# Optimization experiments

Hardware: AMD Instinct MI355X
Metric: run time of the kernel (lower is better)

Reference implementation:

```python
import jax, jax.numpy as jnp
import numpy as np

B, S, V, E, P, C = 256, 128, 32000, 300, 200, 3
DIST_CUTOFF = 10

def _seq_mask(x):
    # TF: count_nonzero over seq, sequence_mask, expand to [B, S, 1]
    size = jnp.sum(x != 0, axis=1)
    m = (jnp.arange(S)[None, :] < size[:, None]).astype(jnp.float32)
    return m[:, :, None]

def _l2norm(w):
    n = jnp.sqrt(jnp.maximum(jnp.sum(w * w, axis=-1, keepdims=True), 1e-12))
    return w / n

def setup_inputs() -> dict:
    key = jax.random.key(0)
    ks = jax.random.split(key, 11)
    std = 0.01
    x1 = jax.random.randint(ks[0], (B, S), 0, V, dtype=jnp.int32)
    x2 = jax.random.randint(ks[1], (B, S), 0, V, dtype=jnp.int32)
    emb = jax.random.normal(ks[2], (V, E), jnp.float32)
    w_intra = jax.random.normal(ks[3], (E, E), jnp.float32) * std
    bias_intra = jax.random.normal(ks[4], (1,), jnp.float32) * std
    w_proj1 = jax.random.normal(ks[5], (2 * E, P), jnp.float32) * std
    w_proj2 = jax.random.normal(ks[6], (2 * E, P), jnp.float32) * std
    w_att = jax.random.normal(ks[7], (P, P), jnp.float32) * std
    w_cmp1 = jax.random.normal(ks[8], (2 * P, 2 * P), jnp.float32) * std
    w_cmp2 = jax.random.normal(ks[9], (2 * P, 2 * P), jnp.float32) * std
    w_agg = jax.random.normal(ks[10], (4 * P, C), jnp.float32) * std
    return dict(x1=x1, x2=x2, emb=emb, w_intra=w_intra, bias_intra=bias_intra,
                w_proj1=w_proj1, w_proj2=w_proj2, w_att=w_att,
                w_cmp1=w_cmp1, w_cmp2=w_cmp2, w_agg=w_agg)

def reference(x1, x2, emb, w_intra, bias_intra, w_proj1, w_proj2, w_att, w_cmp1, w_cmp2, w_agg):
    relu = jax.nn.relu
    mask1, mask2 = _seq_mask(x1), _seq_mask(x2)  # [B,S,1]

    # normalized embedding lookup
    e = _l2norm(emb)
    e1, e2 = e[x1], e[x2]  # [B,S,E]

    # intra-attention with distance bias (bias zeroed for |i-j| < 10)
    idx = jnp.arange(S)
    dist = jnp.abs(idx[None, :] - idx[:, None])
    dbias = bias_intra[0] * (dist >= DIST_CUTOFF).astype(jnp.float32)  # [S,S]

    def intra(x):
        f = relu(x @ w_intra)                       # shared F, [B,S,E]
        att = jnp.einsum('bik,bjk->bij', f, f)      # [B,S,S]
        sm = jax.nn.softmax(att + dbias[None], axis=2)
        xp = jnp.einsum('bik,bkj->bij', sm, x)
        return jnp.concatenate([x, xp], axis=2)     # [B,S,2E]

    e1, e2 = intra(e1), intra(e2)

    # project
    x1p = relu(e1 @ w_proj1)  # [B,S,P]
    x2p = relu(e2 @ w_proj2)

    # attend: F(x1) . F(x2), multiplicative mask, two softmaxes
    f1 = relu(x1p @ w_att)
    f2 = relu(x2p @ w_att)
    sim = jnp.einsum('bik,bjk->bij', f1, f2)          # [B,S1,S2]
    sim = sim * (mask1 * jnp.swapaxes(mask2, 1, 2))   # multiplicative mask (as in source)
    alpha = jnp.einsum('bki,bkj->bij', jax.nn.softmax(sim, axis=1), x1p)  # [B,S2,P]
    beta = jnp.einsum('bik,bkj->bij', jax.nn.softmax(sim, axis=2), x2p)   # [B,S1,P]

    # compare
    v1 = relu(jnp.concatenate([x1p, beta], axis=2) @ w_cmp1)
    v2 = relu(jnp.concatenate([x2p, alpha], axis=2) @ w_cmp2)

    # aggregate (masked sum pooling) + final ReLU projection (faithful to source)
    v1 = jnp.sum(v1 * mask1, axis=1)
    v2 = jnp.sum(v2 * mask2, axis=1)
    y_hat = relu(jnp.concatenate([v1, v2], axis=1) @ w_agg)  # [B,C]
    return y_hat
```

## Files before the change

### kernel.cpp

```cpp
#include <hip/hip_runtime.h>

#define BATCH 256
#define SEQ   128
#define EDIM  300
#define PDIM  200
#define BSTOK (BATCH * SEQ)

#define F_RELU  1
#define F_ACCUM 2

typedef unsigned short u16;
typedef __attribute__((ext_vector_type(8))) short bf16x8;
typedef __attribute__((ext_vector_type(4))) float f32x4;

__device__ __forceinline__ u16 f2bf(float x) {
    unsigned u = __float_as_uint(x);
    unsigned r = u + 0x7fffu + ((u >> 16) & 1u);
    return (u16)(r >> 16);
}
__device__ __forceinline__ float bf2f(u16 h) {
    return __uint_as_float(((unsigned)h) << 16);
}

__device__ __forceinline__ unsigned char* swz16(unsigned char* base, int row, int chunk) {
    return base + row * 64 + (((chunk ^ (row >> 1)) & 3) << 4);
}

__device__ __forceinline__ void split_store8(const float* va,
    unsigned char* bH, unsigned char* bL, int row, int chunk)
{
    unsigned hp[4], lp[4];
    #pragma unroll
    for (int i = 0; i < 4; i++) {
        const unsigned u0 = __float_as_uint(va[2 * i]);
        const unsigned u1 = __float_as_uint(va[2 * i + 1]);
        const unsigned h0 = u0 & 0xffff0000u;
        const unsigned h1 = u1 & 0xffff0000u;
        hp[i] = (u0 >> 16) | h1;
        const float r0 = va[2 * i]     - __uint_as_float(h0);
        const float r1 = va[2 * i + 1] - __uint_as_float(h1);
        lp[i] = (__float_as_uint(r0) >> 16) | (__float_as_uint(r1) & 0xffff0000u);
    }
    *(uint4*)swz16(bH, row, chunk) = make_uint4(hp[0], hp[1], hp[2], hp[3]);
    *(uint4*)swz16(bL, row, chunk) = make_uint4(lp[0], lp[1], lp[2], lp[3]);
}

__device__ __forceinline__ void hi_store8(const float* va,
    unsigned char* bH, int row, int chunk)
{
    unsigned hp[4];
    #pragma unroll
    for (int i = 0; i < 4; i++)
        hp[i] = (unsigned)f2bf(va[2 * i]) | ((unsigned)f2bf(va[2 * i + 1]) << 16);
    *(uint4*)swz16(bH, row, chunk) = make_uint4(hp[0], hp[1], hp[2], hp[3]);
}

__device__ __forceinline__ void gload8(float* va, const float* __restrict__ src,
                                       bool ok)
{
    if (ok) {
        const float4 v0 = *(const float4*)(src);
        const float4 v1 = *(const float4*)(src + 4);
        va[0] = v0.x; va[1] = v0.y; va[2] = v0.z; va[3] = v0.w;
        va[4] = v1.x; va[5] = v1.y; va[6] = v1.z; va[7] = v1.w;
    } else {
        #pragma unroll
        for (int i = 0; i < 8; i++) va[i] = 0.f;
    }
}

__device__ __forceinline__ void kmask8(float* va, int kbase, int Kvalid)
{
    #pragma unroll
    for (int i = 0; i < 8; i++)
        va[i] = (kbase + i < Kvalid) ? va[i] : 0.f;
}

__device__ __forceinline__ void gather8(float* va, const float* __restrict__ erow,
                                        float nrm, int kb)
{
    if (kb + 8 <= EDIM) {
        const float4 v0 = *(const float4*)(erow + kb);
        const float4 v1 = *(const float4*)(erow + kb + 4);
        va[0] = v0.x; va[1] = v0.y; va[2] = v0.z; va[3] = v0.w;
        va[4] = v1.x; va[5] = v1.y; va[6] = v1.z; va[7] = v1.w;
    } else {
        #pragma unroll
        for (int i = 0; i < 8; i++)
            va[i] = (kb + i < EDIM) ? erow[kb + i] : 0.f;
    }
    #pragma unroll
    for (int i = 0; i < 8; i++) va[i] *= nrm;
}

#define MFMA3(ai, aj) \
    acc[ai][aj] = __builtin_amdgcn_mfma_f32_16x16x32_bf16(fah[ai], fbh[aj], acc[ai][aj], 0, 0, 0); \
    acc[ai][aj] = __builtin_amdgcn_mfma_f32_16x16x32_bf16(fah[ai], fbl[aj], acc[ai][aj], 0, 0, 0); \
    acc[ai][aj] = __builtin_amdgcn_mfma_f32_16x16x32_bf16(fal[ai], fbh[aj], acc[ai][aj], 0, 0, 0);

#define MFMA1(ai, aj) \
    acc[ai][aj] = __builtin_amdgcn_mfma_f32_16x16x32_bf16(fah[ai], fbh[aj], acc[ai][aj], 0, 0, 0);


__device__ __forceinline__ void store_transposed(
    float* __restrict__ PT, const f32x4 (*acc)[2], float* TR,
    int bn, int Nvalid, int wr, int wc, int lr, int quad, int tid, bool relu)
{
    #pragma unroll
    for (int h = 0; h < 2; h++) {
        __syncthreads();
        if ((wc >> 6) == h) {
            #pragma unroll
            for (int j = 0; j < 2; j++) {
                const int col = (wc & 63) + j * 16 + lr;
                #pragma unroll
                for (int i = 0; i < 4; i++)
                    #pragma unroll
                    for (int r = 0; r < 4; r++) {
                        float v = acc[i][j][r];
                        if (relu) v = fmaxf(v, 0.f);
                        TR[col * 129 + wr + i * 16 + quad * 4 + r] = v;
                    }
            }
        }
        __syncthreads();
        const int row = tid >> 3;
        const int gp = bn + h * 64 + row;
        if (gp < Nvalid) {
            float* dst = PT + (long long)gp * 128;
            for (int c = (tid & 7); c < 32; c += 8) {
                const int base = row * 129 + c * 4;
                *(float4*)(dst + c * 4) =
                    make_float4(TR[base], TR[base + 1], TR[base + 2], TR[base + 3]);
            }
        }
    }
}

__global__ __launch_bounds__(512, 4) void gemm_proj(
    const int* __restrict__ x1, const int* __restrict__ x2,
    const float* __restrict__ emb, const float* __restrict__ norms,
    const u16* __restrict__ W1h, const u16* __restrict__ W1l,
    const u16* __restrict__ W2h, const u16* __restrict__ W2l,
    float* __restrict__ T, float* __restrict__ F0, float* __restrict__ F1)
{
    __shared__ __align__(16) unsigned char smem[33280];

    const int tid = threadIdx.x;
    const int id  = blockIdx.y * 5 + blockIdx.x;
    const int xcd = id & 7;
    const int s   = id >> 3;
    const int mt  = xcd + 8 * (s / 5);
    const int bm  = mt * 128;
    const int bn  = (s % 5) * 128;
    const bool side2 = mt >= 256;
    const bool wb = bn < 256;

    const u16* Bh = side2 ? W2h : W1h;
    const u16* Bl = side2 ? W2l : W1l;
    float* F = side2 ? F1 : F0;
    const int fm = side2 ? bm - 32768 : bm;
    const int* toks = (side2 ? x2 - 32768 : x1) + bm;

    const int wave = tid >> 6;
    const int lane = tid & 63;
    const int wr   = (wave >> 2) * 64;
    const int wc   = (wave & 3) * 32;
    const int lr   = lane & 15;
    const int quad = lane >> 4;
    const int sr   = tid >> 2;
    const int q    = tid & 3;
    const int scf  = q * 8;

    const int tok = toks[sr];
    const float nrm = norms[tok];
    const float* erow = emb + (long long)tok * EDIM;

    const int gn = bn + sr;
    const bool bok = gn < 556;
    const u16* Bhp = Bh + (long long)gn * 320 + scf;
    const u16* Blp = Bl + (long long)gn * 320 + scf;

    f32x4 acc[4][2];
    #pragma unroll
    for (int i = 0; i < 4; i++)
        #pragma unroll
        for (int j = 0; j < 2; j++)
            acc[i][j] = (f32x4)(0.0f);

    for (int t = 0; t < 10; ++t) {
        float av[8];
        gather8(av, erow, nrm, t * 32 + scf);
        const uint4 bh = bok ? *(const uint4*)(Bhp + t * 32) : make_uint4(0,0,0,0);
        if (wb) {
            const uint4 bl = bok ? *(const uint4*)(Blp + t * 32) : make_uint4(0,0,0,0);
            split_store8(av, smem, smem + 8192, sr, q);
            *(uint4*)swz16(smem + 16384, sr, q) = bh;
            *(uint4*)swz16(smem + 24576, sr, q) = bl;
        } else {
            hi_store8(av, smem, sr, q);
            *(uint4*)swz16(smem + 16384, sr, q) = bh;
        }
        __syncthreads();

        bf16x8 fah[4], fbh[2];
        #pragma unroll
        for (int i = 0; i < 4; i++)
            fah[i] = *(const bf16x8*)swz16(smem, wr + i * 16 + lr, quad);
        #pragma unroll
        for (int j = 0; j < 2; j++)
            fbh[j] = *(const bf16x8*)swz16(smem + 16384, wc + j * 16 + lr, quad);
        if (wb) {
            bf16x8 fal[4], fbl[2];
            #pragma unroll
            for (int i = 0; i < 4; i++)
                fal[i] = *(const bf16x8*)swz16(smem + 8192, wr + i * 16 + lr, quad);
            #pragma unroll
            for (int j = 0; j < 2; j++)
                fbl[j] = *(const bf16x8*)swz16(smem + 24576, wc + j * 16 + lr, quad);
            #pragma unroll
            for (int i = 0; i < 4; i++)
                #pragma unroll
                for (int j = 0; j < 2; j++) { MFMA3(i, j) }
        } else {
            #pragma unroll
            for (int i = 0; i < 4; i++)
                #pragma unroll
                for (int j = 0; j < 2; j++) { MFMA1(i, j) }
        }
        __syncthreads();
    }

    if (wb) {
        float* Tb = T + (long long)mt * (PDIM * SEQ);
        store_transposed(Tb, acc, (float*)smem, bn, PDIM, wr, wc, lr, quad, tid, false);
    } else {
        #pragma unroll
        for (int i = 0; i < 4; i++) {
            #pragma unroll
            for (int j = 0; j < 2; j++) {
                const int idx = bn + wc + j * 16 + lr - 256;
                if (idx >= EDIM) continue;
                #pragma unroll
                for (int r = 0; r < 4; r++) {
                    const int gm = fm + wr + i * 16 + quad * 4 + r;
                    F[(long long)gm * EDIM + idx] = fmaxf(acc[i][j][r], 0.f);
                }
            }
        }
    }
}

__global__ __launch_bounds__(512, 4) void gemm_xp(
    const float* __restrict__ P, float* __restrict__ T,
    const int* __restrict__ x1, const int* __restrict__ x2,
    const float* __restrict__ emb, const float* __restrict__ norms,
    const u16* __restrict__ W1h, const u16* __restrict__ W1l,
    const u16* __restrict__ W2h, const u16* __restrict__ W2l,
    float* __restrict__ XCAT)
{
    __shared__ __align__(16) unsigned char smem[33280];

    const int tid = threadIdx.x;
    const int bz  = blockIdx.z;
    const int bn  = blockIdx.x * 128;

    const int wave = tid >> 6;
    const int lane = tid & 63;
    const int wr   = (wave >> 2) * 64;
    const int wc   = (wave & 3) * 32;
    const int lr   = lane & 15;
    const int quad = lane >> 4;
    const int sr   = tid >> 2;
    const int q    = tid & 3;
    const int scf  = q * 8;

    const int* toks = (bz < BATCH) ? x1 + bz * SEQ : x2 + (bz - BATCH) * SEQ;
    const u16* Wh = (bz < BATCH) ? W1h : W2h;
    const u16* Wl = (bz < BATCH) ? W1l : W2l;
    const int tok = toks[sr];
    const float nrm = norms[tok];
    const float* erow = emb + (long long)tok * EDIM;
    const float* Pb = P + (long long)bz * (SEQ * SEQ);
    float* Tb = T + (long long)bz * (PDIM * SEQ);

    const int gn = bn + sr;
    const bool bok = gn < PDIM;
    const u16* Whp = Wh + (long long)gn * 320 + scf;
    const u16* Wlp = Wl + (long long)gn * 320 + scf;
    const float* Pp = Pb + (long long)sr * 128 + scf;
    const float* Tp = Tb + (long long)gn * 128 + scf;

    f32x4 acc[4][2];
    #pragma unroll
    for (int i = 0; i < 4; i++)
        #pragma unroll
        for (int j = 0; j < 2; j++)
            acc[i][j] = (f32x4)(0.0f);

    for (int t = 0; t < 14; ++t) {
        if (t < 10) {
            float av[8];
            gather8(av, erow, nrm, t * 32 + scf);
            const uint4 bh = bok ? *(const uint4*)(Whp + t * 32) : make_uint4(0,0,0,0);
            const uint4 bl = bok ? *(const uint4*)(Wlp + t * 32) : make_uint4(0,0,0,0);
            split_store8(av, smem, smem + 8192, sr, q);
            *(uint4*)swz16(smem + 16384, sr, q) = bh;
            *(uint4*)swz16(smem + 24576, sr, q) = bl;
        } else {
            float av[8], bv[8];
            gload8(av, Pp + (t - 10) * 32, true);
            gload8(bv, Tp + (t - 10) * 32, bok);
            split_store8(av, smem,         smem + 8192,  sr, q);
            split_store8(bv, smem + 16384, smem + 24576, sr, q);
        }
        __syncthreads();

        bf16x8 fah[4], fal[4], fbh[2], fbl[2];
        #pragma unroll
        for (int i = 0; i < 4; i++) {
            fah[i] = *(const bf16x8*)swz16(smem,        wr + i * 16 + lr, quad);
            fal[i] = *(const bf16x8*)swz16(smem + 8192, wr + i * 16 + lr, quad);
        }
        #pragma unroll
        for (int j = 0; j < 2; j++) {
            fbh[j] = *(const bf16x8*)swz16(smem + 16384, wc + j * 16 + lr, quad);
            fbl[j] = *(const bf16x8*)swz16(smem + 24576, wc + j * 16 + lr, quad);
        }
        #pragma unroll
        for (int i = 0; i < 4; i++)
            #pragma unroll
            for (int j = 0; j < 2; j++) { MFMA3(i, j) }
        __syncthreads();
    }

    const long long rowbase = (long long)bz * SEQ;
    #pragma unroll
    for (int i = 0; i < 4; i++) {
        #pragma unroll
        for (int j = 0; j < 2; j++) {
            const int gnn = bn + wc + j * 16 + lr;
            if (gnn >= PDIM) continue;
            #pragma unroll
            for (int r = 0; r < 4; r++) {
                const int gm = wr + i * 16 + quad * 4 + r;
                XCAT[(rowbase + gm) * 400 + gnn] = fmaxf(acc[i][j][r], 0.f);
            }
        }
    }
    store_transposed(Tb, acc, (float*)smem, bn, PDIM, wr, wc, lr, quad, tid, true);
}

template <int NM>
__global__ __launch_bounds__(512, 4) void gemm_flat(
    const float* __restrict__ A,
    const u16* __restrict__ Bh, const u16* __restrict__ Bl,
    const u16* __restrict__ Bh2, const u16* __restrict__ Bl2, int Msplit,
    float* __restrict__ C, float* __restrict__ PO, const int* __restrict__ sizes,
    int M, int N, int Kp, int lda, int ldb, int ldc, int flags)
{
    constexpr int BOFF = (NM == 3) ? 16384 : 8192;
    __shared__ __align__(16) unsigned char smem[(NM == 3) ? 32768 : 16384];

    const int tid = threadIdx.x;
    int bx = blockIdx.x, by = blockIdx.y;
    if ((gridDim.y & 7) == 0) {
        const int gx = gridDim.x;
        const int id = by * gx + bx;
        const int xcd = id & 7;
        const int s = id >> 3;
        by = xcd + 8 * (s / gx);
        bx = s % gx;
    }
    const int bm = by * 128;
    const int bn = bx * 128;

    const int wave = tid >> 6;
    const int lane = tid & 63;
    const int wr   = (wave >> 2) * 64;
    const int wc   = (wave & 3) * 32;
    const int lr   = lane & 15;
    const int quad = lane >> 4;
    const int sr   = tid >> 2;
    const int q    = tid & 3;
    const int scf  = q * 8;

    if (bm >= Msplit) { Bh = Bh2; Bl = Bl2; }

    const float* Ap = A + (long long)(bm + sr) * lda + scf;
    const int gn = bn + sr;
    const bool bok = gn < N;
    const u16* Bhp = Bh + (long long)gn * ldb + scf;
    const u16* Blp = Bl + (long long)gn * ldb + scf;

    f32x4 acc[4][2];
    #pragma unroll
    for (int i = 0; i < 4; i++)
        #pragma unroll
        for (int j = 0; j < 2; j++)
            acc[i][j] = (f32x4)(0.0f);

    const int NT = Kp >> 5;
    for (int t = 0; t < NT; ++t) {
        float av[8];
        gload8(av, Ap + t * 32, true);
        const uint4 bh = bok ? *(const uint4*)(Bhp + t * 32) : make_uint4(0,0,0,0);
        if constexpr (NM == 3) {
            const uint4 bl = bok ? *(const uint4*)(Blp + t * 32) : make_uint4(0,0,0,0);
            split_store8(av, smem, smem + 8192, sr, q);
            *(uint4*)swz16(smem + BOFF,        sr, q) = bh;
            *(uint4*)swz16(smem + BOFF + 8192, sr, q) = bl;
        } else {
            hi_store8(av, smem, sr, q);
            *(uint4*)swz16(smem + BOFF, sr, q) = bh;
        }
        __syncthreads();

        bf16x8 fah[4], fbh[2];
        #pragma unroll
        for (int i = 0; i < 4; i++)
            fah[i] = *(const bf16x8*)swz16(smem, wr + i * 16 + lr, quad);
        #pragma unroll
        for (int j = 0; j < 2; j++)
            fbh[j] = *(const bf16x8*)swz16(smem + BOFF, wc + j * 16 + lr, quad);
        if constexpr (NM == 3) {
            bf16x8 fal[4], fbl[2];
            #pragma unroll
            for (int i = 0; i < 4; i++)
                fal[i] = *(const bf16x8*)swz16(smem + 8192, wr + i * 16 + lr, quad);
            #pragma unroll
            for (int j = 0; j < 2; j++)
                fbl[j] = *(const bf16x8*)swz16(smem + BOFF + 8192, wc + j * 16 + lr, quad);
            #pragma unroll
            for (int i = 0; i < 4; i++)
                #pragma unroll
                for (int j = 0; j < 2; j++) { MFMA3(i, j) }
        } else {
            #pragma unroll
            for (int i = 0; i < 4; i++)
                #pragma unroll
                for (int j = 0; j < 2; j++) { MFMA1(i, j) }
        }
        __syncthreads();
    }

    const int sz = PO ? sizes[bm >> 7] : 0;
    float ps[2] = {0.f, 0.f};
    #pragma unroll
    for (int j = 0; j < 2; j++) {
        const int gnn = bn + wc + j * 16 + lr;
        const bool gok = gnn < N;
        #pragma unroll
        for (int i = 0; i < 4; i++) {
            #pragma unroll
            for (int r = 0; r < 4; r++) {
                const int row = wr + i * 16 + quad * 4 + r;
                const int gm = bm + row;
                float v = acc[i][j][r];
                if (flags & F_RELU) v = fmaxf(v, 0.f);
                if (gok && C) C[(long long)gm * ldc + gnn] = v;
                if (PO && row < sz) ps[j] += v;
            }
        }
    }
    if (PO) {
        #pragma unroll
        for (int j = 0; j < 2; j++) {
            ps[j] += __shfl_xor(ps[j], 16);
            ps[j] += __shfl_xor(ps[j], 32);
        }
        float* PS = (float*)smem;
        __syncthreads();
        if (wr == 0 && quad == 0) {
            #pragma unroll
            for (int j = 0; j < 2; j++) PS[wc + j * 16 + lr] = ps[j];
        }
        __syncthreads();
        if (wr == 64 && quad == 0) {
            #pragma unroll
            for (int j = 0; j < 2; j++) PS[wc + j * 16 + lr] += ps[j];
        }
        __syncthreads();
        if (tid < 128) {
            const int gnn = bn + tid;
            if (gnn < N) PO[(long long)(bm >> 7) * N + gnn] = PS[tid];
        }
    }
}

#define SLD 132
template <int MODE>
__global__ __launch_bounds__(512, (MODE == 0) ? 4 : 2) void gemm_bat(
    const float* __restrict__ A, const float* __restrict__ Aalt,
    const float* __restrict__ B, const float* __restrict__ Balt,
    float* __restrict__ C, float* __restrict__ PT,
    int N, int Kvalid, int Kp, int lda, int ldb, int ldc,
    long long sA, long long sB, long long sC, long long sPT,
    int flags, const float* __restrict__ bias_ptr, const int* __restrict__ sizes,
    int same_ab)
{
    constexpr int NM = (MODE == 0) ? 3 : 1;
    constexpr int BOFF = (NM == 3) ? 16384 : 8192;
    constexpr int SMB  = (MODE == 0) ? 32768 : (128 * SLD * 4);
    __shared__ __align__(16) unsigned char smem[SMB];

    const int bz = blockIdx.z;
    long long zb = bz;
    const float* Ause = A;
    const float* Buse = B;
    if (Aalt && bz >= BATCH) { Ause = Aalt; Buse = Balt; zb = bz - BATCH; }
    Ause += zb * sA;
    Buse += zb * sB;
    C += (long long)bz * sC;
    if (PT) PT += (long long)bz * sPT;

    const int tid  = threadIdx.x;
    const int bn   = blockIdx.x * 128;
    const int wave = tid >> 6;
    const int lane = tid & 63;
    const int wr   = (wave >> 2) * 64;
    const int wc   = (wave & 3) * 32;
    const int lr   = lane & 15;
    const int quad = lane >> 4;
    const int sr   = tid >> 2;
    const int q    = tid & 3;
    const int scf  = q * 8;

    f32x4 acc[4][2];
    #pragma unroll
    for (int i = 0; i < 4; i++)
        #pragma unroll
        for (int j = 0; j < 2; j++)
            acc[i][j] = (f32x4)(0.0f);

    const float* Apt = Ause + (long long)sr * lda + scf;
    const int gn = bn + sr;
    const bool bok = gn < N;
    const float* Bpt = Buse + (long long)gn * ldb + scf;

    const int NT = Kp >> 5;
    for (int t = 0; t < NT; ++t) {
        float av[8];
        gload8(av, Apt + t * 32, true);
        kmask8(av, t * 32 + scf, Kvalid);
        if constexpr (NM == 3) split_store8(av, smem, smem + 8192, sr, q);
        else                   hi_store8(av, smem, sr, q);
        if (!same_ab) {
            float bv[8];
            gload8(bv, Bpt + t * 32, bok);
            kmask8(bv, t * 32 + scf, Kvalid);
            if constexpr (NM == 3) split_store8(bv, smem + BOFF, smem + BOFF + 8192, sr, q);
            else                   hi_store8(bv, smem + BOFF, sr, q);
        }
        __syncthreads();

        unsigned char* rbB = same_ab ? smem : smem + BOFF;
        bf16x8 fah[4], fbh[2];
        #pragma unroll
        for (int i = 0; i < 4; i++)
            fah[i] = *(const bf16x8*)swz16(smem, wr + i * 16 + lr, quad);
        #pragma unroll
        for (int j = 0; j < 2; j++)
            fbh[j] = *(const bf16x8*)swz16(rbB, wc + j * 16 + lr, quad);
        if constexpr (NM == 3) {
            bf16x8 fal[4], fbl[2];
            #pragma unroll
            for (int i = 0; i < 4; i++)
                fal[i] = *(const bf16x8*)swz16(smem + 8192, wr + i * 16 + lr, quad);
            #pragma unroll
            for (int j = 0; j < 2; j++)
                fbl[j] = *(const bf16x8*)swz16(rbB + 8192, wc + j * 16 + lr, quad);
            #pragma unroll
            for (int i = 0; i < 4; i++)
                #pragma unroll
                for (int j = 0; j < 2; j++) { MFMA3(i, j) }
        } else {
            #pragma unroll
            for (int i = 0; i < 4; i++)
                #pragma unroll
                for (int j = 0; j < 2; j++) { MFMA1(i, j) }
        }
        __syncthreads();
    }

    if (MODE == 1) {
        float* S = (float*)smem;
        const float bias = bias_ptr[0];
        #pragma unroll
        for (int i = 0; i < 4; i++) {
            #pragma unroll
            for (int j = 0; j < 2; j++) {
                const int col = wc + j * 16 + lr;
                #pragma unroll
                for (int r = 0; r < 4; r++) {
                    const int row = wr + i * 16 + quad * 4 + r;
                    int d = row - col; d = d < 0 ? -d : d;
                    S[row * SLD + col] = acc[i][j][r] + ((d >= 10) ? bias : 0.f);
                }
            }
        }
        __syncthreads();
        const int row = tid >> 2;
        const int qd  = (tid & 3) * 32;
        float* Sr = S + row * SLD + qd;
        float mx = -1e30f;
        #pragma unroll
        for (int c = 0; c < 8; c++) {
            const float4 v = *(const float4*)(Sr + c * 4);
            mx = fmaxf(fmaxf(fmaxf(mx, v.x), fmaxf(v.y, v.z)), v.w);
        }
        mx = fmaxf(mx, __shfl_xor(mx, 1));
        mx = fmaxf(mx, __shfl_xor(mx, 2));
        float sum = 0.f;
        #pragma unroll
        for (int c = 0; c < 8; c++) {
            float4 v = *(const float4*)(Sr + c * 4);
            v.x = __expf(v.x - mx); v.y = __expf(v.y - mx);
            v.z = __expf(v.z - mx); v.w = __expf(v.w - mx);
            sum += (v.x + v.y) + (v.z + v.w);
            *(float4*)(Sr + c * 4) = v;
        }
        sum += __shfl_xor(sum, 1);
        sum += __shfl_xor(sum, 2);
        const float inv = 1.f / sum;
        #pragma unroll
        for (int c = 0; c < 8; c++) {
            float4 v = *(const float4*)(Sr + c * 4);
            v.x *= inv; v.y *= inv; v.z *= inv; v.w *= inv;
            *(float4*)&C[(long long)row * ldc + qd + c * 4] = v;
        }
    } else if (MODE == 2) {
        float* S = (float*)smem;
        const int s1 = sizes[bz];
        const int s2 = sizes[BATCH + bz];
        #pragma unroll
        for (int i = 0; i < 4; i++) {
            #pragma unroll
            for (int j = 0; j < 2; j++) {
                const int col = wc + j * 16 + lr;
                #pragma unroll
                for (int r = 0; r < 4; r++) {
                    const int row = wr + i * 16 + quad * 4 + r;
                    float v = acc[i][j][r];
                    if (row >= s1 || col >= s2) v = 0.f;
                    S[row * SLD + col] = v;
                }
            }
        }
        __syncthreads();
        const int row = tid >> 2;
        const int qd  = (tid & 3) * 32;
        {
            const float* Sr = S + row * SLD + qd;
            float mx = -1e30f;
            #pragma unroll
            for (int c = 0; c < 8; c++) {
                const float4 v = *(const float4*)(Sr + c * 4);
                mx = fmaxf(fmaxf(fmaxf(mx, v.x), fmaxf(v.y, v.z)), v.w);
            }
            mx = fmaxf(mx, __shfl_xor(mx, 1));
            mx = fmaxf(mx, __shfl_xor(mx, 2));
            float sum = 0.f;
            #pragma unroll
            for (int c = 0; c < 8; c++) {
                const float4 v = *(const float4*)(Sr + c * 4);
                sum += (__expf(v.x - mx) + __expf(v.y - mx))
                     + (__expf(v.z - mx) + __expf(v.w - mx));
            }
            sum += __shfl_xor(sum, 1);
            sum += __shfl_xor(sum, 2);
            const float inv = 1.f / sum;
            #pragma unroll
            for (int c = 0; c < 8; c++) {
                const float4 v = *(const float4*)(Sr + c * 4);
                float4 o;
                o.x = __expf(v.x - mx) * inv; o.y = __expf(v.y - mx) * inv;
                o.z = __expf(v.z - mx) * inv; o.w = __expf(v.w - mx) * inv;
                *(float4*)&C[(long long)row * 128 + qd + c * 4] = o;
            }
        }
        {
            const int colx = row;
            float mx = -1e30f;
            for (int r = 0; r < 32; r++)
                mx = fmaxf(mx, S[(qd + r) * SLD + colx]);
            mx = fmaxf(mx, __shfl_xor(mx, 1));
            mx = fmaxf(mx, __shfl_xor(mx, 2));
            float sum = 0.f;
            for (int r = 0; r < 32; r++)
                sum += __expf(S[(qd + r) * SLD + colx] - mx);
            sum += __shfl_xor(sum, 1);
            sum += __shfl_xor(sum, 2);
            const float inv = 1.f / sum;
            #pragma unroll
            for (int r4 = 0; r4 < 8; r4++) {
                float4 o;
                o.x = __expf(S[(qd + r4 * 4 + 0) * SLD + colx] - mx) * inv;
                o.y = __expf(S[(qd + r4 * 4 + 1) * SLD + colx] - mx) * inv;
                o.z = __expf(S[(qd + r4 * 4 + 2) * SLD + colx] - mx) * inv;
                o.w = __expf(S[(qd + r4 * 4 + 3) * SLD + colx] - mx) * inv;
                *(float4*)&PT[(long long)colx * 128 + qd + r4 * 4] = o;
            }
        }
    } else {
        const int s1 = sizes ? sizes[bz] : SEQ;
        const int s2 = sizes ? sizes[BATCH + bz] : SEQ;
        #pragma unroll
        for (int i = 0; i < 4; i++) {
            #pragma unroll
            for (int j = 0; j < 2; j++) {
                const int gnn = bn + wc + j * 16 + lr;
                if (gnn >= N) continue;
                #pragma unroll
                for (int r = 0; r < 4; r++) {
                    const int gm = wr + i * 16 + quad * 4 + r;
                    float v = acc[i][j][r];
                    if (sizes && (gm >= s1 || gnn >= s2)) v = 0.f;
                    if (flags & F_ACCUM) v += C[(long long)gm * ldc + gnn];
                    if (flags & F_RELU)  v = fmaxf(v, 0.f);
                    C[(long long)gm * ldc + gnn] = v;
                    if (PT) PT[(long long)gnn * 128 + gm] = v;
                }
            }
        }
    }
}

struct WEnt { const float* src; u16* H; u16* L; int K, N, Kp, rowStart; };
struct WTab { WEnt e[11]; };
__global__ void convert_all(WTab t)
{
    const int row = blockIdx.y;
    const int k = blockIdx.x * 256 + threadIdx.x;
    #pragma unroll
    for (int s = 0; s < 11; s++) {
        const WEnt w = t.e[s];
        if (row >= w.rowStart && row < w.rowStart + w.N) {
            const int n = row - w.rowStart;
            if (k < w.Kp) {
                const float v = (k < w.K) ? w.src[(long long)k * w.N + n] : 0.f;
                const u16 h = f2bf(v);
                w.H[(long long)n * w.Kp + k] = h;
                w.L[(long long)n * w.Kp + k] = f2bf(v - bf2f(h));
            }
            return;
        }
    }
}

__global__ void norms_kernel(const float* __restrict__ emb, float* __restrict__ norms)
{
    const int r = blockIdx.x;
    const int lane = threadIdx.x;
    const float* row = emb + (long long)r * EDIM;
    float ss = 0.f;
    #pragma unroll
    for (int i = 0; i < 5; i++) {
        const int c = lane + i * 64;
        const float f = (c < EDIM) ? row[c] : 0.f;
        ss += f * f;
    }
    #pragma unroll
    for (int o = 32; o > 0; o >>= 1) ss += __shfl_xor(ss, o);
    if (lane == 0) norms[r] = rsqrtf(fmaxf(ss, 1e-12f));
}

__global__ void sizes_kernel(const int* __restrict__ x1, const int* __restrict__ x2,
                             int* __restrict__ sizes)
{
    const int b = blockIdx.x;
    const int side = blockIdx.y;
    const int* x = (side ? x2 : x1) + b * SEQ;
    const int nz = (x[threadIdx.x] != 0) ? 1 : 0;
    const unsigned long long bal = __ballot(nz);
    __shared__ int part[2];
    if ((threadIdx.x & 63) == 0) part[threadIdx.x >> 6] = __popcll(bal);
    __syncthreads();
    if (threadIdx.x == 0) sizes[side * BATCH + b] = part[0] + part[1];
}

__global__ void agg_kernel(const float* __restrict__ v1s, const float* __restrict__ v2s,
                           const float* __restrict__ w_agg, float* __restrict__ y)
{
    const int b = blockIdx.x;
    const int lane = threadIdx.x;
    float a0 = 0.f, a1 = 0.f, a2 = 0.f;
    for (int k = lane; k < 800; k += 64) {
        const float v = (k < 400) ? v1s[b * 400 + k] : v2s[b * 400 + k - 400];
        a0 = fmaf(v, w_agg[k * 3 + 0], a0);
        a1 = fmaf(v, w_agg[k * 3 + 1], a1);
        a2 = fmaf(v, w_agg[k * 3 + 2], a2);
    }
    #pragma unroll
    for (int o = 32; o > 0; o >>= 1) {
        a0 += __shfl_xor(a0, o);
        a1 += __shfl_xor(a1, o);
        a2 += __shfl_xor(a2, o);
    }
    if (lane == 0) {
        y[b * 3 + 0] = fmaxf(a0, 0.f);
        y[b * 3 + 1] = fmaxf(a1, 0.f);
        y[b * 3 + 2] = fmaxf(a2, 0.f);
    }
}

extern "C" void kernel_launch(void* const* d_in, const int* in_sizes, int n_in,
                              void* d_out, int out_size, void* d_ws, size_t ws_size,
                              hipStream_t stream)
{
    (void)in_sizes; (void)n_in; (void)out_size; (void)ws_size;
    const int*   x1         = (const int*)d_in[0];
    const int*   x2         = (const int*)d_in[1];
    const float* emb        = (const float*)d_in[2];
    const float* w_intra    = (const float*)d_in[3];
    const float* bias_intra = (const float*)d_in[4];
    const float* w_proj1    = (const float*)d_in[5];
    const float* w_proj2    = (const float*)d_in[6];
    const float* w_att      = (const float*)d_in[7];
    const float* w_cmp1     = (const float*)d_in[8];
    const float* w_cmp2     = (const float*)d_in[9];
    const float* w_agg      = (const float*)d_in[10];
    float* y  = (float*)d_out;
    float* ws = (float*)d_ws;

    float* X1CAT = ws;
    float* X2CAT = X1CAT + 13107200;
    float* T     = X2CAT + 13107200;
    float* FBUF  = T + 13107200;
    float* ATT   = FBUF + 9830400;
    float* POOL  = ATT + 8388608;
    int*   SIZES = (int*)(POOL + 204800);
    float* NORMS = (float*)(SIZES + 512);
    u16*   W1H   = (u16*)(NORMS + 32768);
    u16*   W1L   = W1H + 177920;
    u16*   W2H   = W1L + 177920;
    u16*   W2L   = W2H + 177920;
    u16*   WAH   = W2L + 177920;
    u16*   WAL   = WAH + 44800;
    u16*   WC1H  = WAL + 44800;
    u16*   WC1L  = WC1H + 166400;
    u16*   WC2H  = WC1L + 166400;
    u16*   WC2L  = WC2H + 166400;
    u16*   WPA1H = WC2L + 166400;
    u16*   WPA1L = WPA1H + 64000;
    u16*   WPA2H = WPA1L + 64000;
    u16*   WPA2L = WPA2H + 64000;

    float* F1X = X1CAT;
    float* F12 = FBUF;
    float* F2  = FBUF + 6553600;
    float* SIMP = F2;
    float* SMTP = F12;
    float* T1  = T;
    float* T2  = T + 6553600;

    const long long sbSS = (long long)SEQ * SEQ;
    const long long sbF  = (long long)SEQ * EDIM;
    const long long sbFP = 25600;
    const long long sbC  = (long long)SEQ * 400;
    const long long sbT  = (long long)PDIM * SEQ;

    sizes_kernel<<<dim3(BATCH, 2), 128, 0, stream>>>(x1, x2, SIZES);
    norms_kernel<<<32000, 64, 0, stream>>>(emb, NORMS);

    {
        WTab t;
        t.e[0]  = { w_proj1 + 300 * 200, W1H,             W1L,             300, 200, 320, 0    };
        t.e[1]  = { w_intra,             W1H + 200 * 320, W1L + 200 * 320,   0,  56, 320, 200  };
        t.e[2]  = { w_intra,             W1H + 256 * 320, W1L + 256 * 320, 300, 300, 320, 256  };
        t.e[3]  = { w_proj2 + 300 * 200, W2H,             W2L,             300, 200, 320, 556  };
        t.e[4]  = { w_intra,             W2H + 200 * 320, W2L + 200 * 320,   0,  56, 320, 756  };
        t.e[5]  = { w_intra,             W2H + 256 * 320, W2L + 256 * 320, 300, 300, 320, 812  };
        t.e[6]  = { w_att,               WAH,             WAL,             200, 200, 224, 1112 };
        t.e[7]  = { w_cmp1,              WC1H,            WC1L,            400, 400, 416, 1312 };
        t.e[8]  = { w_cmp2,              WC2H,            WC2L,            400, 400, 416, 1712 };
        t.e[9]  = { w_proj1,             WPA1H,           WPA1L,           300, 200, 320, 2112 };
        t.e[10] = { w_proj2,             WPA2H,           WPA2L,           300, 200, 320, 2312 };
        convert_all<<<dim3(2, 2512), 256, 0, stream>>>(t);
    }

    gemm_proj<<<dim3(5, 512), 512, 0, stream>>>(
        x1, x2, emb, NORMS, W1H, W1L, W2H, W2L, T, FBUF, F1X);
    gemm_bat<1><<<dim3(1, 1, 2 * BATCH), 512, 0, stream>>>(
        FBUF, F1X, FBUF, nullptr, ATT, nullptr,
        SEQ, EDIM, 320, EDIM, EDIM, SEQ, sbF, sbF, sbSS, 0,
        0, bias_intra, nullptr, 1);
    gemm_xp<<<dim3(2, 1, 2 * BATCH), 512, 0, stream>>>(
        ATT, T, x1, x2, emb, NORMS, WPA1H, WPA1L, WPA2H, WPA2L, X1CAT);

    gemm_flat<1><<<dim3(2, 512), 512, 0, stream>>>(
        X1CAT, WAH, WAL, WAH, WAL, 1 << 30, F12, nullptr, nullptr,
        2 * BSTOK, PDIM, 224, 400, 224, PDIM, F_RELU);
    gemm_bat<2><<<dim3(1, 1, BATCH), 512, 0, stream>>>(
        F12, nullptr, F2, nullptr, SIMP, SMTP,
        SEQ, PDIM, 224, PDIM, PDIM, SEQ, sbFP, sbFP, sbFP, sbFP,
        0, nullptr, SIZES, 0);
    gemm_bat<0><<<dim3(2, 1, 2 * BATCH), 512, 0, stream>>>(
        SIMP, SMTP, T2, T1, X1CAT + 200, nullptr,
        PDIM, SEQ, SEQ, SEQ, SEQ, 400, sbFP, sbT, sbC, 0,
        0, nullptr, nullptr, 0);

    gemm_flat<3><<<dim3(4, 512), 512, 0, stream>>>(
        X1CAT, WC1H, WC1L, WC2H, WC2L, BSTOK,
        nullptr, POOL, SIZES,
        2 * BSTOK, 400, 416, 400, 416, 400, F_RELU);
    agg_kernel<<<BATCH, 64, 0, stream>>>(POOL, POOL + 102400, w_agg, y);
}
```

Baseline: 478.4 us.

## Prefetch next K-tile global loads into registers across GEMM kernels

Across the four GEMM-style kernels, the next K-tile's global loads are now issued into registers before the barrier and MFMA compute of the current tile, instead of at the start of each iteration. This is meant to hide global memory latency behind the MFMA work without adding an LDS buffer. The embedding norm scaling moves to store time so the raw row can be prefetched. The cost is higher register pressure, which may reduce occupancy.

```diff
diff --git a/kernel.cpp b/kernel.cpp
--- a/kernel.cpp
+++ b/kernel.cpp
@@ -69,15 +69,8 @@
     }
 }
 
-__device__ __forceinline__ void kmask8(float* va, int kbase, int Kvalid)
-{
-    #pragma unroll
-    for (int i = 0; i < 8; i++)
-        va[i] = (kbase + i < Kvalid) ? va[i] : 0.f;
-}
-
-__device__ __forceinline__ void gather8(float* va, const float* __restrict__ erow,
-                                        float nrm, int kb)
+__device__ __forceinline__ void gload_emb8(float* va, const float* __restrict__ erow,
+                                           int kb)
 {
     if (kb + 8 <= EDIM) {
         const float4 v0 = *(const float4*)(erow + kb);
@@ -89,8 +82,13 @@
         for (int i = 0; i < 8; i++)
             va[i] = (kb + i < EDIM) ? erow[kb + i] : 0.f;
     }
-    #pragma unroll
-    for (int i = 0; i < 8; i++) va[i] *= nrm;
+}
+
+__device__ __forceinline__ void kmask8(float* va, int kbase, int Kvalid)
+{
+    #pragma unroll
+    for (int i = 0; i < 8; i++)
+        va[i] = (kbase + i < Kvalid) ? va[i] : 0.f;
 }
 
 #define MFMA3(ai, aj) \
@@ -188,18 +186,26 @@
         for (int j = 0; j < 2; j++)
             acc[i][j] = (f32x4)(0.0f);
 
+    float av[8];
+    uint4 bh, bl;
+    gload_emb8(av, erow, scf);
+    bh = bok ? *(const uint4*)(Bhp) : make_uint4(0,0,0,0);
+    if (wb) bl = bok ? *(const uint4*)(Blp) : make_uint4(0,0,0,0);
+
     for (int t = 0; t < 10; ++t) {
-        float av[8];
-        gather8(av, erow, nrm, t * 32 + scf);
-        const uint4 bh = bok ? *(const uint4*)(Bhp + t * 32) : make_uint4(0,0,0,0);
-        if (wb) {
-            const uint4 bl = bok ? *(const uint4*)(Blp + t * 32) : make_uint4(0,0,0,0);
-            split_store8(av, smem, smem + 8192, sr, q);
+        {
+            float sv[8];
+            #pragma unroll
+            for (int i = 0; i < 8; i++) sv[i] = av[i] * nrm;
+            if (wb) split_store8(sv, smem, smem + 8192, sr, q);
+            else    hi_store8(sv, smem, sr, q);
             *(uint4*)swz16(smem + 16384, sr, q) = bh;
-            *(uint4*)swz16(smem + 24576, sr, q) = bl;
-        } else {
-            hi_store8(av, smem, sr, q);
-            *(uint4*)swz16(smem + 16384, sr, q) = bh;
+            if (wb) *(uint4*)swz16(smem + 24576, sr, q) = bl;
+        }
+        if (t < 9) {
+            gload_emb8(av, erow, (t + 1) * 32 + scf);
+            bh = bok ? *(const uint4*)(Bhp + (t + 1) * 32) : make_uint4(0,0,0,0);
+            if (wb) bl = bok ? *(const uint4*)(Blp + (t + 1) * 32) : make_uint4(0,0,0,0);
         }
         __syncthreads();
 
@@ -298,22 +304,35 @@
         for (int j = 0; j < 2; j++)
             acc[i][j] = (f32x4)(0.0f);
 
+    float av[8], bv[8];
+    uint4 bh, bl;
+
+#define XP_LOAD(sidx) do { \
+    if ((sidx) < 10) { \
+        gload_emb8(av, erow, (sidx) * 32 + scf); \
+        bh = bok ? *(const uint4*)(Whp + (sidx) * 32) : make_uint4(0,0,0,0); \
+        bl = bok ? *(const uint4*)(Wlp + (sidx) * 32) : make_uint4(0,0,0,0); \
+    } else { \
+        gload8(av, Pp + ((sidx) - 10) * 32, true); \
+        gload8(bv, Tp + ((sidx) - 10) * 32, bok); \
+    } \
+} while (0)
+
+    XP_LOAD(0);
+
     for (int t = 0; t < 14; ++t) {
         if (t < 10) {
-            float av[8];
-            gather8(av, erow, nrm, t * 32 + scf);
-            const uint4 bh = bok ? *(const uint4*)(Whp + t * 32) : make_uint4(0,0,0,0);
-            const uint4 bl = bok ? *(const uint4*)(Wlp + t * 32) : make_uint4(0,0,0,0);
-            split_store8(av, smem, smem + 8192, sr, q);
+            float sv[8];
+            #pragma unroll
+            for (int i = 0; i < 8; i++) sv[i] = av[i] * nrm;
+            split_store8(sv, smem, smem + 8192, sr, q);
             *(uint4*)swz16(smem + 16384, sr, q) = bh;
             *(uint4*)swz16(smem + 24576, sr, q) = bl;
         } else {
-            float av[8], bv[8];
-            gload8(av, Pp + (t - 10) * 32, true);
-            gload8(bv, Tp + (t - 10) * 32, bok);
             split_store8(av, smem,         smem + 8192,  sr, q);
             split_store8(bv, smem + 16384, smem + 24576, sr, q);
         }
+        if (t < 13) XP_LOAD(t + 1);
         __syncthreads();
 
         bf16x8 fah[4], fal[4], fbh[2], fbl[2];
@@ -333,6 +352,7 @@
             for (int j = 0; j < 2; j++) { MFMA3(i, j) }
         __syncthreads();
     }
+#undef XP_LOAD
 
     const long long rowbase = (long long)bz * SEQ;
     #pragma unroll
@@ -401,18 +421,26 @@
             acc[i][j] = (f32x4)(0.0f);
 
     const int NT = Kp >> 5;
+    float av[8];
+    uint4 bh, bl;
+    gload8(av, Ap, true);
+    bh = bok ? *(const uint4*)(Bhp) : make_uint4(0,0,0,0);
+    if constexpr (NM == 3) bl = bok ? *(const uint4*)(Blp) : make_uint4(0,0,0,0);
+
     for (int t = 0; t < NT; ++t) {
-        float av[8];
-        gload8(av, Ap + t * 32, true);
-        const uint4 bh = bok ? *(const uint4*)(Bhp + t * 32) : make_uint4(0,0,0,0);
         if constexpr (NM == 3) {
-            const uint4 bl = bok ? *(const uint4*)(Blp + t * 32) : make_uint4(0,0,0,0);
             split_store8(av, smem, smem + 8192, sr, q);
             *(uint4*)swz16(smem + BOFF,        sr, q) = bh;
             *(uint4*)swz16(smem + BOFF + 8192, sr, q) = bl;
         } else {
             hi_store8(av, smem, sr, q);
             *(uint4*)swz16(smem + BOFF, sr, q) = bh;
+        }
+        if (t < NT - 1) {
+            gload8(av, Ap + (t + 1) * 32, true);
+            bh = bok ? *(const uint4*)(Bhp + (t + 1) * 32) : make_uint4(0,0,0,0);
+            if constexpr (NM == 3)
+                bl = bok ? *(const uint4*)(Blp + (t + 1) * 32) : make_uint4(0,0,0,0);
         }
         __syncthreads();
 
@@ -539,18 +567,22 @@
     const float* Bpt = Buse + (long long)gn * ldb + scf;
 
     const int NT = Kp >> 5;
+    float av[8], bv[8];
+    gload8(av, Apt, true);
+    if (!same_ab) gload8(bv, Bpt, bok);
+
     for (int t = 0; t < NT; ++t) {
-        float av[8];
-        gload8(av, Apt + t * 32, true);
         kmask8(av, t * 32 + scf, Kvalid);
         if constexpr (NM == 3) split_store8(av, smem, smem + 8192, sr, q);
         else                   hi_store8(av, smem, sr, q);
         if (!same_ab) {
-            float bv[8];
-            gload8(bv, Bpt + t * 32, bok);
             kmask8(bv, t * 32 + scf, Kvalid);
             if constexpr (NM == 3) split_store8(bv, smem + BOFF, smem + BOFF + 8192, sr, q);
             else                   hi_store8(bv, smem + BOFF, sr, q);
+        }
+        if (t < NT - 1) {
+            gload8(av, Apt + (t + 1) * 32, true);
+            if (!same_ab) gload8(bv, Bpt + (t + 1) * 32, bok);
         }
         __syncthreads();
 
```

Result: faster. 462.1 us (-3.4%).
